# Kernel optimization log

Measured on AMD Instinct MI355X. Metric: run time of the kernel, lower is better.

Reference implementation:

```python
import jax, jax.numpy as jnp
import numpy as np

EPS = 1e-5  # torch BatchNorm2d default eps

def _bn(x, gamma, beta):
    # training-mode batch statistics over (N,H,W), per channel (biased variance)
    mean = jnp.mean(x, axis=(0, 2, 3), keepdims=True)
    var = jnp.var(x, axis=(0, 2, 3), keepdims=True)
    return gamma[None, :, None, None] * (x - mean) * jax.lax.rsqrt(var + EPS) + beta[None, :, None, None]

def _conv1x1(x, w, b):
    # (B,C,H,W) x (O,C) -> (B,O,H,W)
    return jnp.einsum('bchw,oc->bohw', x, w) + b[None, :, None, None]

def _maxpool2(x):
    B, C, H, W = x.shape
    return x.reshape(B, C, H // 2, 2, W // 2, 2).max(axis=(3, 5))

def setup_inputs() -> dict:
    key = jax.random.key(0)
    ks = jax.random.split(key, 5)
    B, C, H, W = 16, 256, 56, 56
    Ci, Cg = C // 8, C // 4
    def kaiming(k, o, i):
        return jax.random.normal(k, (o, i), jnp.float32) * np.float32(np.sqrt(2.0 / i))
    return {
        'x': jax.random.normal(ks[0], (B, C, H, W), jnp.float32),
        'bn1_gamma': jnp.ones((C,), jnp.float32),
        'bn1_beta': jnp.zeros((C,), jnp.float32),
        'w_g': kaiming(ks[1], Cg, C), 'b_g': jnp.zeros((Cg,), jnp.float32),
        'w_theta': kaiming(ks[2], Ci, C), 'b_theta': jnp.zeros((Ci,), jnp.float32),
        'w_phi': kaiming(ks[3], Ci, C), 'b_phi': jnp.zeros((Ci,), jnp.float32),
        'bn2_gamma': jnp.ones((Cg,), jnp.float32),
        'bn2_beta': jnp.zeros((Cg,), jnp.float32),
        'w_z': kaiming(ks[4], C, Cg), 'b_z': jnp.zeros((C,), jnp.float32),
    }

def reference(x, bn1_gamma, bn1_beta, w_g, b_g, w_theta, b_theta, w_phi, b_phi, bn2_gamma, bn2_beta, w_z, b_z):
    identity = x
    B, C, H, W = x.shape
    xa = jax.nn.relu(_bn(x, bn1_gamma, bn1_beta))
    g_x = _maxpool2(_conv1x1(xa, w_g, b_g))        # (B,Cg,H/2,W/2)
    phi_x = _maxpool2(_conv1x1(xa, w_phi, b_phi))  # (B,Ci,H/2,W/2)
    theta_x = _conv1x1(xa, w_theta, b_theta)       # (B,Ci,H,W)
    Cg = g_x.shape[1]
    Ci = theta_x.shape[1]
    Np = g_x.shape[2] * g_x.shape[3]               # subsampled positions (H/2*W/2)
    g_x = g_x.reshape(B, Cg, Np).transpose(0, 2, 1)      # (B,Np,Cg)
    phi_x = phi_x.reshape(B, Ci, Np)                     # (B,Ci,Np)
    theta_x = theta_x.reshape(B, Ci, H * W).transpose(0, 2, 1)  # (B,HW,Ci)
    f_div_C = jnp.einsum('bnc,bcm->bnm', theta_x, phi_x) / Np   # (B,HW,Np)
    y = jnp.einsum('bnm,bmc->bnc', f_div_C, g_x)                # (B,HW,Cg)
    y = y.transpose(0, 2, 1).reshape(B, Cg, H, W)
    w_y = _conv1x1(jax.nn.relu(_bn(y, bn2_gamma, bn2_beta)), w_z, b_z)
    return w_y + identity
```

## Files before the change

### kernel.cpp

```cpp
#include <hip/hip_runtime.h>
#include <hip/hip_bf16.h>

#define BB 16
#define CC 256
#define HWN 3136
#define NCG 64
#define NCI 32
#define NPP 784

typedef __attribute__((ext_vector_type(8))) short short8;
typedef __attribute__((ext_vector_type(4))) float floatx4;

__device__ __forceinline__ unsigned short f2bf(float f) {
    union { __hip_bfloat16 h; unsigned short u; } cv;
    cv.h = __float2bfloat16(f);
    return cv.u;
}
__device__ __forceinline__ float bf2f(unsigned short u) {
    return __uint_as_float(((unsigned)u) << 16);
}

__global__ __launch_bounds__(256) void k_prep(const float* __restrict__ w_t,
                                              const float* __restrict__ w_p,
                                              const float* __restrict__ w_g,
                                              const float* __restrict__ w_z,
                                              unsigned short* __restrict__ wcat,
                                              unsigned short* __restrict__ wzb,
                                              float* __restrict__ accs) {
    int o = blockIdx.x;
    int c = threadIdx.x;
    const float* src = (o < 32) ? (w_t + o * CC)
                      : (o < 64) ? (w_p + (o - 32) * CC)
                                 : (w_g + (o - 64) * CC);
    wcat[o * CC + c] = f2bf(src[c]);
    {
        int r = o * 2 + (c >> 7);
        int kk = c & 127;
        if (kk < 72)
            wzb[r * 72 + kk] = (kk < 64) ? f2bf(w_z[r * 64 + kk]) : (unsigned short)0;
    }
    if (o == 0) {
        for (int i = c; i < 640; i += 256) accs[i] = 0.f;
    }
}

__global__ __launch_bounds__(256) void k_bn1a(const float* __restrict__ x,
                                              float* __restrict__ acc) {
    int blk = blockIdx.x;
    int c = blk & (CC - 1);
    const float4* p = (const float4*)(x + (size_t)blk * HWN);
    int tid = threadIdx.x;
    float s = 0.f, q = 0.f;
    #pragma unroll
    for (int i = tid; i < 784; i += 256) {
        float4 v = p[i];
        s += v.x + v.y + v.z + v.w;
        q += v.x * v.x + v.y * v.y + v.z * v.z + v.w * v.w;
    }
    #pragma unroll
    for (int off = 32; off > 0; off >>= 1) {
        s += __shfl_down(s, off);
        q += __shfl_down(q, off);
    }
    __shared__ float sh[8];
    int wid = tid >> 6, lane = tid & 63;
    if (lane == 0) { sh[wid] = s; sh[4 + wid] = q; }
    __syncthreads();
    if (tid == 0) {
        atomicAdd(&acc[c], sh[0] + sh[1] + sh[2] + sh[3]);
        atomicAdd(&acc[CC + c], sh[4] + sh[5] + sh[6] + sh[7]);
    }
}

__global__ __launch_bounds__(256) void k_conv1(const float* __restrict__ x,
                                               const unsigned short* __restrict__ wcat,
                                               const float* __restrict__ bn1acc,
                                               const float* __restrict__ gamma,
                                               const float* __restrict__ beta,
                                               const float* __restrict__ b_g,
                                               const float* __restrict__ b_t,
                                               const float* __restrict__ b_p,
                                               unsigned short* __restrict__ conv1) {
    int b = blockIdx.y;
    int hw0 = blockIdx.x * 64;
    int tid = threadIdx.x;
    int wv = tid >> 6, ln = tid & 63;

    __shared__ unsigned short Asmem[128 * 32];
    __shared__ unsigned short Bsmem[64 * 32];
    __shared__ float ab_s[512];
    __shared__ float bias_s[128];

    {
        const float inv = 1.0f / (BB * HWN);
        float mean = bn1acc[tid] * inv;
        float var  = bn1acc[CC + tid] * inv - mean * mean;
        float a = gamma[tid] * rsqrtf(var + 1e-5f);
        ab_s[tid] = a;
        ab_s[CC + tid] = beta[tid] - mean * a;
    }
    if (tid < 128) {
        int o = tid;
        bias_s[o] = (o < 32) ? b_t[o] : (o < 64) ? b_p[o - 32] : b_g[o - 64];
    }
    __syncthreads();

    floatx4 acc[2][4];
    #pragma unroll
    for (int mt = 0; mt < 2; ++mt)
        for (int nt = 0; nt < 4; ++nt)
            acc[mt][nt] = (floatx4){0.f, 0.f, 0.f, 0.f};

    int p   = tid & 15;
    int hwq = tid >> 4;
    const float* xb = x + (size_t)(b * CC) * HWN + hw0 + hwq * 4;

    int col = ln & 15, quad = ln >> 4;

    for (int k0 = 0; k0 < CC; k0 += 32) {
        #pragma unroll
        for (int i = 0; i < 2; ++i) {
            int row = wv * 32 + i * 16 + (ln >> 2);
            int q   = ln & 3;
            const unsigned short* gp = wcat + row * CC + k0 + q * 8;
            __builtin_amdgcn_global_load_lds(
                (const __attribute__((address_space(1))) unsigned int*)gp,
                (__attribute__((address_space(3))) unsigned int*)&Asmem[(wv * 2 + i) * 512],
                16, 0, 0);
        }
        {
            int c0 = k0 + 2 * p;
            float4 v0 = *(const float4*)(xb + (size_t)c0 * HWN);
            float4 v1 = *(const float4*)(xb + (size_t)(c0 + 1) * HWN);
            float a0 = ab_s[c0],     d0 = ab_s[CC + c0];
            float a1 = ab_s[c0 + 1], d1 = ab_s[CC + c0 + 1];
            float r0[4] = { fmaxf(fmaf(a0, v0.x, d0), 0.f), fmaxf(fmaf(a0, v0.y, d0), 0.f),
                            fmaxf(fmaf(a0, v0.z, d0), 0.f), fmaxf(fmaf(a0, v0.w, d0), 0.f) };
            float r1[4] = { fmaxf(fmaf(a1, v1.x, d1), 0.f), fmaxf(fmaf(a1, v1.y, d1), 0.f),
                            fmaxf(fmaf(a1, v1.z, d1), 0.f), fmaxf(fmaf(a1, v1.w, d1), 0.f) };
            unsigned int* bw = (unsigned int*)Bsmem;
            #pragma unroll
            for (int i = 0; i < 4; ++i) {
                unsigned int w = (unsigned int)f2bf(r0[i]) | ((unsigned int)f2bf(r1[i]) << 16);
                bw[(hwq * 4 + i) * 16 + p] = w;
            }
        }
        __syncthreads();

        short8 af0 = *(const short8*)&Asmem[(wv * 32 +      (ln & 15)) * 32 + quad * 8];
        short8 af1 = *(const short8*)&Asmem[(wv * 32 + 16 + (ln & 15)) * 32 + quad * 8];
        #pragma unroll
        for (int nt = 0; nt < 4; ++nt) {
            short8 bf = *(const short8*)&Bsmem[(nt * 16 + (ln & 15)) * 32 + quad * 8];
            acc[0][nt] = __builtin_amdgcn_mfma_f32_16x16x32_bf16(af0, bf, acc[0][nt], 0, 0, 0);
            acc[1][nt] = __builtin_amdgcn_mfma_f32_16x16x32_bf16(af1, bf, acc[1][nt], 0, 0, 0);
        }
        __syncthreads();
    }

    #pragma unroll
    for (int mt = 0; mt < 2; ++mt) {
        int obase = wv * 32 + mt * 16 + quad * 4;
        #pragma unroll
        for (int r = 0; r < 4; ++r) {
            int o = obase + r;
            float bias = bias_s[o];
            #pragma unroll
            for (int nt = 0; nt < 4; ++nt) {
                float val = acc[mt][nt][r] + bias;
                conv1[((size_t)(b * 128 + o)) * HWN + hw0 + nt * 16 + col] = f2bf(val);
            }
        }
    }
}

__global__ __launch_bounds__(256) void k_spart(const unsigned short* __restrict__ conv1,
                                               float* __restrict__ spart) {
    int cx = blockIdx.x;
    int b  = blockIdx.y;
    int tid = threadIdx.x;
    __shared__ float pl[96 * 60];

    #pragma unroll
    for (int i = 0; i < 21; ++i) {
        int e = tid + i * 256;
        int ch = e / 56, mm = e - ch * 56;
        int m = cx * 56 + mm;
        int mh = m / 28, mw = m - mh * 28;
        const unsigned short* p = conv1 + ((size_t)(b * 128 + 32 + ch)) * HWN + mh * 112 + mw * 2;
        pl[ch * 60 + mm] = fmaxf(fmaxf(bf2f(p[0]), bf2f(p[1])),
                                 fmaxf(bf2f(p[56]), bf2f(p[57])));
    }
    __syncthreads();

    int cg = tid & 63;
    int cib = tid >> 6;
    float acc[8];
    #pragma unroll
    for (int i = 0; i < 8; ++i) acc[i] = 0.f;
    const float* pb = &pl[(32 + cg) * 60];
    for (int mm4 = 0; mm4 < 14; ++mm4) {
        float4 bv = *(const float4*)&pb[mm4 * 4];
        #pragma unroll
        for (int i = 0; i < 8; ++i) {
            float4 av = *(const float4*)&pl[(cib + 4 * i) * 60 + mm4 * 4];
            acc[i] = fmaf(av.x, bv.x, acc[i]);
            acc[i] = fmaf(av.y, bv.y, acc[i]);
            acc[i] = fmaf(av.z, bv.z, acc[i]);
            acc[i] = fmaf(av.w, bv.w, acc[i]);
        }
    }
    float* out = spart + ((size_t)(b * 14 + cx)) * 2048;
    #pragma unroll
    for (int i = 0; i < 8; ++i) out[tid + i * 256] = acc[i];
}

__global__ __launch_bounds__(256) void k_y(const unsigned short* __restrict__ conv1,
                                           const float* __restrict__ spart,
                                           unsigned short* __restrict__ y,
                                           float* __restrict__ bn2acc) {
    int b = blockIdx.y;
    int hw0 = blockIdx.x * 64;
    int tid = threadIdx.x;
    int wv = tid >> 6, ln = tid & 63;
    int col = ln & 15, quad = ln >> 4;

    __shared__ unsigned short St[64 * 40];
    __shared__ unsigned short Tt[64 * 40];
    __shared__ float shs[64], shq[64];

    for (int id = tid; id < 2048; id += 256) {
        const float* p = spart + (size_t)b * 14 * 2048 + id;
        float s = 0.f;
        #pragma unroll
        for (int j = 0; j < 14; ++j) s += p[j * 2048];
        int ci = id >> 6, cg = id & 63;
        St[cg * 40 + ci] = f2bf(s * (1.0f / NPP));
    }
    {
        int p2 = tid & 15, hwq = tid >> 4;
        int c0 = 2 * p2;
        const unsigned short* tb = conv1 + (size_t)(b * 128) * HWN + hw0 + hwq * 4;
        ushort4 v0 = *(const ushort4*)(tb + (size_t)c0 * HWN);
        ushort4 v1 = *(const ushort4*)(tb + (size_t)(c0 + 1) * HWN);
        unsigned int* tw = (unsigned int*)Tt;
        tw[(hwq * 4 + 0) * 20 + p2] = (unsigned)v0.x | ((unsigned)v1.x << 16);
        tw[(hwq * 4 + 1) * 20 + p2] = (unsigned)v0.y | ((unsigned)v1.y << 16);
        tw[(hwq * 4 + 2) * 20 + p2] = (unsigned)v0.z | ((unsigned)v1.z << 16);
        tw[(hwq * 4 + 3) * 20 + p2] = (unsigned)v0.w | ((unsigned)v1.w << 16);
    }
    if (tid < 64) { shs[tid] = 0.f; shq[tid] = 0.f; }
    __syncthreads();

    short8 af = *(const short8*)&Tt[(wv * 16 + col) * 40 + quad * 8];
    #pragma unroll
    for (int nt = 0; nt < 4; ++nt) {
        short8 bf = *(const short8*)&St[(nt * 16 + col) * 40 + quad * 8];
        floatx4 acc = (floatx4){0.f, 0.f, 0.f, 0.f};
        acc = __builtin_amdgcn_mfma_f32_16x16x32_bf16(af, bf, acc, 0, 0, 0);
        int cg = nt * 16 + col;
        int hw = hw0 + wv * 16 + quad * 4;
        ushort4 st;
        st.x = f2bf(acc[0]); st.y = f2bf(acc[1]);
        st.z = f2bf(acc[2]); st.w = f2bf(acc[3]);
        *(ushort4*)&y[((size_t)(b * NCG + cg)) * HWN + hw] = st;
        float s = acc[0] + acc[1] + acc[2] + acc[3];
        float q = acc[0] * acc[0] + acc[1] * acc[1] + acc[2] * acc[2] + acc[3] * acc[3];
        atomicAdd(&shs[cg], s);
        atomicAdd(&shq[cg], q);
    }
    __syncthreads();
    if (tid < 64) {
        atomicAdd(&bn2acc[tid], shs[tid]);
        atomicAdd(&bn2acc[64 + tid], shq[tid]);
    }
}

__global__ __launch_bounds__(256) void k_convz(const unsigned short* __restrict__ y,
                                               const unsigned short* __restrict__ wzb,
                                               const float* __restrict__ bn2acc,
                                               const float* __restrict__ gamma,
                                               const float* __restrict__ beta,
                                               const float* __restrict__ b_z,
                                               const float* __restrict__ x,
                                               float* __restrict__ out) {
    int b = blockIdx.y;
    int hw0 = blockIdx.x * 64;
    int tid = threadIdx.x;
    int wv = tid >> 6, ln = tid & 63;
    int col = ln & 15, quad = ln >> 4;

    __shared__ unsigned short Wl[256 * 72];
    __shared__ unsigned short Yt[64 * 72];
    __shared__ float ab2_s[128];

    #pragma unroll
    for (int i = 0; i < 9; ++i) {
        int j = wv * 9 + i;
        const unsigned short* gp = wzb + j * 512 + ln * 8;
        __builtin_amdgcn_global_load_lds(
            (const __attribute__((address_space(1))) unsigned int*)gp,
            (__attribute__((address_space(3))) unsigned int*)&Wl[j * 512],
            16, 0, 0);
    }
    if (tid < 64) {
        const float inv = 1.0f / (BB * HWN);
        float mean = bn2acc[tid] * inv;
        float var  = bn2acc[64 + tid] * inv - mean * mean;
        float a = gamma[tid] * rsqrtf(var + 1e-5f);
        ab2_s[tid] = a;
        ab2_s[64 + tid] = beta[tid] - mean * a;
    }
    __syncthreads();

    {
        int p2 = tid & 15, hwq = tid >> 4;
        const unsigned short* ybase = y + (size_t)(b * NCG) * HWN + hw0 + hwq * 4;
        unsigned int* yw = (unsigned int*)Yt;
        #pragma unroll
        for (int h = 0; h < 2; ++h) {
            int k0 = h * 32 + 2 * p2;
            ushort4 v0 = *(const ushort4*)(ybase + (size_t)k0 * HWN);
            ushort4 v1 = *(const ushort4*)(ybase + (size_t)(k0 + 1) * HWN);
            float a0 = ab2_s[k0],     d0 = ab2_s[64 + k0];
            float a1 = ab2_s[k0 + 1], d1 = ab2_s[64 + k0 + 1];
            float r0[4] = { fmaxf(fmaf(a0, bf2f(v0.x), d0), 0.f), fmaxf(fmaf(a0, bf2f(v0.y), d0), 0.f),
                            fmaxf(fmaf(a0, bf2f(v0.z), d0), 0.f), fmaxf(fmaf(a0, bf2f(v0.w), d0), 0.f) };
            float r1[4] = { fmaxf(fmaf(a1, bf2f(v1.x), d1), 0.f), fmaxf(fmaf(a1, bf2f(v1.y), d1), 0.f),
                            fmaxf(fmaf(a1, bf2f(v1.z), d1), 0.f), fmaxf(fmaf(a1, bf2f(v1.w), d1), 0.f) };
            #pragma unroll
            for (int i = 0; i < 4; ++i) {
                unsigned int w = (unsigned int)f2bf(r0[i]) | ((unsigned int)f2bf(r1[i]) << 16);
                yw[(hwq * 4 + i) * 36 + h * 16 + p2] = w;
            }
        }
    }
    __syncthreads();

    floatx4 acc[16];
    #pragma unroll
    for (int nt = 0; nt < 16; ++nt) acc[nt] = (floatx4){0.f, 0.f, 0.f, 0.f};

    #pragma unroll
    for (int kk = 0; kk < 2; ++kk) {
        short8 af = *(const short8*)&Yt[(wv * 16 + col) * 72 + kk * 32 + quad * 8];
        #pragma unroll
        for (int nt = 0; nt < 16; ++nt) {
            short8 bf = *(const short8*)&Wl[(nt * 16 + col) * 72 + kk * 32 + quad * 8];
            acc[nt] = __builtin_amdgcn_mfma_f32_16x16x32_bf16(af, bf, acc[nt], 0, 0, 0);
        }
    }

    #pragma unroll
    for (int nt = 0; nt < 16; ++nt) {
        int co = nt * 16 + col;
        size_t base = ((size_t)(b * CC + co)) * HWN + hw0 + wv * 16 + quad * 4;
        float4 xv = *(const float4*)&x[base];
        float bz = b_z[co];
        float4 r = make_float4(acc[nt][0] + bz + xv.x, acc[nt][1] + bz + xv.y,
                               acc[nt][2] + bz + xv.z, acc[nt][3] + bz + xv.w);
        *(float4*)&out[base] = r;
    }
}

extern "C" void kernel_launch(void* const* d_in, const int* in_sizes, int n_in,
                              void* d_out, int out_size, void* d_ws, size_t ws_size,
                              hipStream_t stream) {
    (void)in_sizes; (void)n_in; (void)out_size; (void)ws_size;
    const float* x   = (const float*)d_in[0];
    const float* g1  = (const float*)d_in[1];
    const float* b1  = (const float*)d_in[2];
    const float* w_g = (const float*)d_in[3];
    const float* b_g = (const float*)d_in[4];
    const float* w_t = (const float*)d_in[5];
    const float* b_t = (const float*)d_in[6];
    const float* w_p = (const float*)d_in[7];
    const float* b_p = (const float*)d_in[8];
    const float* g2  = (const float*)d_in[9];
    const float* b2  = (const float*)d_in[10];
    const float* w_z = (const float*)d_in[11];
    const float* b_z = (const float*)d_in[12];
    float* out = (float*)d_out;

    float* ws     = (float*)d_ws;
    float* bn1acc = ws;
    float* bn2acc = ws + 512;
    unsigned short* wcat  = (unsigned short*)(ws + 1024);
    unsigned short* wzb   = (unsigned short*)(ws + 17408);
    unsigned short* conv1 = (unsigned short*)(ws + 26624);
    float* spart  = ws + 3237888;
    unsigned short* yb    = (unsigned short*)(ws + 3696640);

    k_prep  <<<dim3(128),       dim3(256), 0, stream>>>(w_t, w_p, w_g, w_z, wcat, wzb, ws);
    k_bn1a  <<<dim3(BB * CC),   dim3(256), 0, stream>>>(x, bn1acc);
    k_conv1 <<<dim3(49, BB),    dim3(256), 0, stream>>>(x, wcat, bn1acc, g1, b1, b_g, b_t, b_p, conv1);
    k_spart <<<dim3(14, BB),    dim3(256), 0, stream>>>(conv1, spart);
    k_y     <<<dim3(49, BB),    dim3(256), 0, stream>>>(conv1, spart, yb, bn2acc);
    k_convz <<<dim3(49, BB),    dim3(256), 0, stream>>>(yb, wzb, bn2acc, g2, b2, b_z, x, out);
}
```

Before: 198.8 us.

## Fuse maxpool into conv1 epilogue and compute pooled phi-g product with MFMA

conv1 now tiles 112 positions (two image rows) per block. This lets it apply the 2x2 maxpool in its epilogue through shared memory and write only theta and the pooled phi/g tensors, with the pooled rows padded to 800 so K-tiles divide evenly. The old scalar k_spart partial-sum kernel plus the 14-way reduction inside k_y are replaced by a per-batch MFMA kernel that writes the final bf16 S matrix directly. This cuts conv1 output traffic and the reduction work, but the new S kernel runs only 16 blocks, which may leave most of the GPU idle.

After: 192.8 us. 1.03x faster.

```diff
diff --git a/kernel.cpp b/kernel.cpp
--- a/kernel.cpp
+++ b/kernel.cpp
@@ -26,6 +26,7 @@
                                               const float* __restrict__ w_z,
                                               unsigned short* __restrict__ wcat,
                                               unsigned short* __restrict__ wzb,
+                                              unsigned short* __restrict__ pool,
                                               float* __restrict__ accs) {
     int o = blockIdx.x;
     int c = threadIdx.x;
@@ -39,6 +40,10 @@
         if (kk < 72)
             wzb[r * 72 + kk] = (kk < 64) ? f2bf(w_z[r * 64 + kk]) : (unsigned short)0;
     }
+    if (o < 96) {
+        int b = c >> 4, kk = c & 15;
+        pool[((size_t)(b * 96 + o)) * 800 + 784 + kk] = 0;
+    }
     if (o == 0) {
         for (int i = c; i < 640; i += 256) accs[i] = 0.f;
     }
@@ -80,14 +85,18 @@
                                                const float* __restrict__ b_g,
                                                const float* __restrict__ b_t,
                                                const float* __restrict__ b_p,
-                                               unsigned short* __restrict__ conv1) {
-    int b = blockIdx.y;
-    int hw0 = blockIdx.x * 64;
+                                               unsigned short* __restrict__ th,
+                                               unsigned short* __restrict__ pool) {
+    int b  = blockIdx.y;
+    int bx = blockIdx.x;
+    int hw0 = bx * 112;
     int tid = threadIdx.x;
     int wv = tid >> 6, ln = tid & 63;
-
-    __shared__ unsigned short Asmem[128 * 32];
-    __shared__ unsigned short Bsmem[64 * 32];
+    int col = ln & 15, quad = ln >> 4;
+
+    __shared__ unsigned short smem[128 * 120];
+    unsigned short* As = smem;
+    unsigned short* Bs = smem + 4096;
     __shared__ float ab_s[512];
     __shared__ float bias_s[128];
 
@@ -105,17 +114,15 @@
     }
     __syncthreads();
 
-    floatx4 acc[2][4];
+    floatx4 acc[2][7];
     #pragma unroll
     for (int mt = 0; mt < 2; ++mt)
-        for (int nt = 0; nt < 4; ++nt)
+        for (int nt = 0; nt < 7; ++nt)
             acc[mt][nt] = (floatx4){0.f, 0.f, 0.f, 0.f};
 
     int p   = tid & 15;
     int hwq = tid >> 4;
-    const float* xb = x + (size_t)(b * CC) * HWN + hw0 + hwq * 4;
-
-    int col = ln & 15, quad = ln >> 4;
+    const float* xb = x + (size_t)(b * CC) * HWN + hw0;
 
     for (int k0 = 0; k0 < CC; k0 += 32) {
         #pragma unroll
@@ -125,98 +132,133 @@
             const unsigned short* gp = wcat + row * CC + k0 + q * 8;
             __builtin_amdgcn_global_load_lds(
                 (const __attribute__((address_space(1))) unsigned int*)gp,
-                (__attribute__((address_space(3))) unsigned int*)&Asmem[(wv * 2 + i) * 512],
+                (__attribute__((address_space(3))) unsigned int*)&As[(wv * 2 + i) * 512],
                 16, 0, 0);
         }
         {
             int c0 = k0 + 2 * p;
-            float4 v0 = *(const float4*)(xb + (size_t)c0 * HWN);
-            float4 v1 = *(const float4*)(xb + (size_t)(c0 + 1) * HWN);
             float a0 = ab_s[c0],     d0 = ab_s[CC + c0];
             float a1 = ab_s[c0 + 1], d1 = ab_s[CC + c0 + 1];
-            float r0[4] = { fmaxf(fmaf(a0, v0.x, d0), 0.f), fmaxf(fmaf(a0, v0.y, d0), 0.f),
-                            fmaxf(fmaf(a0, v0.z, d0), 0.f), fmaxf(fmaf(a0, v0.w, d0), 0.f) };
-            float r1[4] = { fmaxf(fmaf(a1, v1.x, d1), 0.f), fmaxf(fmaf(a1, v1.y, d1), 0.f),
-                            fmaxf(fmaf(a1, v1.z, d1), 0.f), fmaxf(fmaf(a1, v1.w, d1), 0.f) };
-            unsigned int* bw = (unsigned int*)Bsmem;
+            unsigned int* bw = (unsigned int*)Bs;
             #pragma unroll
-            for (int i = 0; i < 4; ++i) {
-                unsigned int w = (unsigned int)f2bf(r0[i]) | ((unsigned int)f2bf(r1[i]) << 16);
-                bw[(hwq * 4 + i) * 16 + p] = w;
+            for (int t = 0; t < 2; ++t) {
+                int qi = hwq + 16 * t;
+                if (qi < 28) {
+                    float4 v0 = *(const float4*)(xb + (size_t)c0 * HWN + qi * 4);
+                    float4 v1 = *(const float4*)(xb + (size_t)(c0 + 1) * HWN + qi * 4);
+                    float r0[4] = { fmaxf(fmaf(a0, v0.x, d0), 0.f), fmaxf(fmaf(a0, v0.y, d0), 0.f),
+                                    fmaxf(fmaf(a0, v0.z, d0), 0.f), fmaxf(fmaf(a0, v0.w, d0), 0.f) };
+                    float r1[4] = { fmaxf(fmaf(a1, v1.x, d1), 0.f), fmaxf(fmaf(a1, v1.y, d1), 0.f),
+                                    fmaxf(fmaf(a1, v1.z, d1), 0.f), fmaxf(fmaf(a1, v1.w, d1), 0.f) };
+                    #pragma unroll
+                    for (int i = 0; i < 4; ++i) {
+                        unsigned int w = (unsigned int)f2bf(r0[i]) | ((unsigned int)f2bf(r1[i]) << 16);
+                        bw[(qi * 4 + i) * 16 + p] = w;
+                    }
+                }
             }
         }
         __syncthreads();
 
-        short8 af0 = *(const short8*)&Asmem[(wv * 32 +      (ln & 15)) * 32 + quad * 8];
-        short8 af1 = *(const short8*)&Asmem[(wv * 32 + 16 + (ln & 15)) * 32 + quad * 8];
-        #pragma unroll
-        for (int nt = 0; nt < 4; ++nt) {
-            short8 bf = *(const short8*)&Bsmem[(nt * 16 + (ln & 15)) * 32 + quad * 8];
+        short8 af0 = *(const short8*)&As[(wv * 32 +      col) * 32 + quad * 8];
+        short8 af1 = *(const short8*)&As[(wv * 32 + 16 + col) * 32 + quad * 8];
+        #pragma unroll
+        for (int nt = 0; nt < 7; ++nt) {
+            short8 bf = *(const short8*)&Bs[(nt * 16 + col) * 32 + quad * 8];
             acc[0][nt] = __builtin_amdgcn_mfma_f32_16x16x32_bf16(af0, bf, acc[0][nt], 0, 0, 0);
             acc[1][nt] = __builtin_amdgcn_mfma_f32_16x16x32_bf16(af1, bf, acc[1][nt], 0, 0, 0);
         }
         __syncthreads();
     }
 
+    unsigned short* Ct = smem;
     #pragma unroll
     for (int mt = 0; mt < 2; ++mt) {
         int obase = wv * 32 + mt * 16 + quad * 4;
         #pragma unroll
         for (int r = 0; r < 4; ++r) {
-            int o = obase + r;
-            float bias = bias_s[o];
+            float bias = bias_s[obase + r];
             #pragma unroll
-            for (int nt = 0; nt < 4; ++nt) {
-                float val = acc[mt][nt][r] + bias;
-                conv1[((size_t)(b * 128 + o)) * HWN + hw0 + nt * 16 + col] = f2bf(val);
+            for (int nt = 0; nt < 7; ++nt)
+                Ct[(obase + r) * 120 + nt * 16 + col] = f2bf(acc[mt][nt][r] + bias);
+        }
+    }
+    __syncthreads();
+
+    #pragma unroll
+    for (int i = 0; i < 4; ++i) {
+        int e = tid + i * 256;
+        if (e < 896) {
+            int ch = e / 28, c4 = e - ch * 28;
+            ushort4 v = *(const ushort4*)&Ct[ch * 120 + c4 * 4];
+            *(ushort4*)&th[((size_t)(b * NCI + ch)) * HWN + hw0 + c4 * 4] = v;
+        }
+    }
+    #pragma unroll
+    for (int i = 0; i < 11; ++i) {
+        int e = tid + i * 256;
+        if (e < 2688) {
+            int ch = e / 28, m = e - ch * 28;
+            const unsigned short* r0p = &Ct[(32 + ch) * 120 + 2 * m];
+            float v = fmaxf(fmaxf(bf2f(r0p[0]), bf2f(r0p[1])),
+                            fmaxf(bf2f(r0p[56]), bf2f(r0p[57])));
+            pool[((size_t)(b * 96 + ch)) * 800 + bx * 28 + m] = f2bf(v);
+        }
+    }
+}
+
+__global__ __launch_bounds__(256) void k_sgemm(const unsigned short* __restrict__ pool,
+                                               unsigned short* __restrict__ Sg) {
+    int b = blockIdx.x;
+    int tid = threadIdx.x;
+    int wv = tid >> 6, ln = tid & 63;
+    int col = ln & 15, quad = ln >> 4;
+    __shared__ float Sred[4 * 2048];
+
+    const unsigned short* gbase = pool + ((size_t)(b * 96 + 32)) * 800;
+    const unsigned short* pbase = pool + ((size_t)(b * 96)) * 800;
+
+    floatx4 acc[4][2];
+    #pragma unroll
+    for (int mt = 0; mt < 4; ++mt)
+        for (int nt = 0; nt < 2; ++nt)
+            acc[mt][nt] = (floatx4){0.f, 0.f, 0.f, 0.f};
+
+    for (int s = wv; s < 25; s += 4) {
+        int k0 = s * 32;
+        short8 af[4], bfr[2];
+        #pragma unroll
+        for (int mt = 0; mt < 4; ++mt)
+            af[mt] = *(const short8*)&gbase[(mt * 16 + col) * 800 + k0 + quad * 8];
+        #pragma unroll
+        for (int nt = 0; nt < 2; ++nt)
+            bfr[nt] = *(const short8*)&pbase[(nt * 16 + col) * 800 + k0 + quad * 8];
+        #pragma unroll
+        for (int mt = 0; mt < 4; ++mt)
+            #pragma unroll
+            for (int nt = 0; nt < 2; ++nt)
+                acc[mt][nt] = __builtin_amdgcn_mfma_f32_16x16x32_bf16(af[mt], bfr[nt], acc[mt][nt], 0, 0, 0);
+    }
+    #pragma unroll
+    for (int mt = 0; mt < 4; ++mt)
+        for (int nt = 0; nt < 2; ++nt)
+            for (int r = 0; r < 4; ++r) {
+                int cg = mt * 16 + quad * 4 + r;
+                int ci = nt * 16 + col;
+                Sred[wv * 2048 + cg * 32 + ci] = acc[mt][nt][r];
             }
-        }
-    }
-}
-
-__global__ __launch_bounds__(256) void k_spart(const unsigned short* __restrict__ conv1,
-                                               float* __restrict__ spart) {
-    int cx = blockIdx.x;
-    int b  = blockIdx.y;
-    int tid = threadIdx.x;
-    __shared__ float pl[96 * 60];
-
-    #pragma unroll
-    for (int i = 0; i < 21; ++i) {
-        int e = tid + i * 256;
-        int ch = e / 56, mm = e - ch * 56;
-        int m = cx * 56 + mm;
-        int mh = m / 28, mw = m - mh * 28;
-        const unsigned short* p = conv1 + ((size_t)(b * 128 + 32 + ch)) * HWN + mh * 112 + mw * 2;
-        pl[ch * 60 + mm] = fmaxf(fmaxf(bf2f(p[0]), bf2f(p[1])),
-                                 fmaxf(bf2f(p[56]), bf2f(p[57])));
-    }
-    __syncthreads();
-
-    int cg = tid & 63;
-    int cib = tid >> 6;
-    float acc[8];
-    #pragma unroll
-    for (int i = 0; i < 8; ++i) acc[i] = 0.f;
-    const float* pb = &pl[(32 + cg) * 60];
-    for (int mm4 = 0; mm4 < 14; ++mm4) {
-        float4 bv = *(const float4*)&pb[mm4 * 4];
-        #pragma unroll
-        for (int i = 0; i < 8; ++i) {
-            float4 av = *(const float4*)&pl[(cib + 4 * i) * 60 + mm4 * 4];
-            acc[i] = fmaf(av.x, bv.x, acc[i]);
-            acc[i] = fmaf(av.y, bv.y, acc[i]);
-            acc[i] = fmaf(av.z, bv.z, acc[i]);
-            acc[i] = fmaf(av.w, bv.w, acc[i]);
-        }
-    }
-    float* out = spart + ((size_t)(b * 14 + cx)) * 2048;
-    #pragma unroll
-    for (int i = 0; i < 8; ++i) out[tid + i * 256] = acc[i];
-}
-
-__global__ __launch_bounds__(256) void k_y(const unsigned short* __restrict__ conv1,
-                                           const float* __restrict__ spart,
+    __syncthreads();
+    #pragma unroll
+    for (int j = 0; j < 8; ++j) {
+        int idx = tid + j * 256;
+        float s = Sred[idx] + Sred[2048 + idx] + Sred[4096 + idx] + Sred[6144 + idx];
+        int cg = idx >> 5, ci = idx & 31;
+        Sg[(size_t)b * 2560 + cg * 40 + ci] = f2bf(s * (1.0f / NPP));
+    }
+}
+
+__global__ __launch_bounds__(256) void k_y(const unsigned short* __restrict__ th,
+                                           const unsigned short* __restrict__ Sg,
                                            unsigned short* __restrict__ y,
                                            float* __restrict__ bn2acc) {
     int b = blockIdx.y;
@@ -229,18 +271,15 @@
     __shared__ unsigned short Tt[64 * 40];
     __shared__ float shs[64], shq[64];
 
-    for (int id = tid; id < 2048; id += 256) {
-        const float* p = spart + (size_t)b * 14 * 2048 + id;
-        float s = 0.f;
-        #pragma unroll
-        for (int j = 0; j < 14; ++j) s += p[j * 2048];
-        int ci = id >> 6, cg = id & 63;
-        St[cg * 40 + ci] = f2bf(s * (1.0f / NPP));
+    {
+        const unsigned int* sgw = (const unsigned int*)(Sg + (size_t)b * 2560);
+        unsigned int* stw = (unsigned int*)St;
+        for (int i = tid; i < 1280; i += 256) stw[i] = sgw[i];
     }
     {
         int p2 = tid & 15, hwq = tid >> 4;
         int c0 = 2 * p2;
-        const unsigned short* tb = conv1 + (size_t)(b * 128) * HWN + hw0 + hwq * 4;
+        const unsigned short* tb = th + (size_t)(b * NCI) * HWN + hw0 + hwq * 4;
         ushort4 v0 = *(const ushort4*)(tb + (size_t)c0 * HWN);
         ushort4 v1 = *(const ushort4*)(tb + (size_t)(c0 + 1) * HWN);
         unsigned int* tw = (unsigned int*)Tt;
@@ -387,14 +426,15 @@
     float* bn2acc = ws + 512;
     unsigned short* wcat  = (unsigned short*)(ws + 1024);
     unsigned short* wzb   = (unsigned short*)(ws + 17408);
-    unsigned short* conv1 = (unsigned short*)(ws + 26624);
-    float* spart  = ws + 3237888;
-    unsigned short* yb    = (unsigned short*)(ws + 3696640);
-
-    k_prep  <<<dim3(128),       dim3(256), 0, stream>>>(w_t, w_p, w_g, w_z, wcat, wzb, ws);
-    k_bn1a  <<<dim3(BB * CC),   dim3(256), 0, stream>>>(x, bn1acc);
-    k_conv1 <<<dim3(49, BB),    dim3(256), 0, stream>>>(x, wcat, bn1acc, g1, b1, b_g, b_t, b_p, conv1);
-    k_spart <<<dim3(14, BB),    dim3(256), 0, stream>>>(conv1, spart);
-    k_y     <<<dim3(49, BB),    dim3(256), 0, stream>>>(conv1, spart, yb, bn2acc);
-    k_convz <<<dim3(49, BB),    dim3(256), 0, stream>>>(yb, wzb, bn2acc, g2, b2, b_z, x, out);
-}
+    unsigned short* th    = (unsigned short*)(ws + 26624);
+    unsigned short* pool  = (unsigned short*)(ws + 829440);
+    unsigned short* Sg    = (unsigned short*)(ws + 1443840);
+    unsigned short* yb    = (unsigned short*)(ws + 1464320);
+
+    k_prep  <<<dim3(128),     dim3(256), 0, stream>>>(w_t, w_p, w_g, w_z, wcat, wzb, pool, ws);
+    k_bn1a  <<<dim3(BB * CC), dim3(256), 0, stream>>>(x, bn1acc);
+    k_conv1 <<<dim3(28, BB),  dim3(256), 0, stream>>>(x, wcat, bn1acc, g1, b1, b_g, b_t, b_p, th, pool);
+    k_sgemm <<<dim3(BB),      dim3(256), 0, stream>>>(pool, Sg);
+    k_y     <<<dim3(49, BB),  dim3(256), 0, stream>>>(th, Sg, yb, bn2acc);
+    k_convz <<<dim3(49, BB),  dim3(256), 0, stream>>>(yb, wzb, bn2acc, g2, b2, b_z, x, out);
+}
```
